# Kernel optimization log

Measured on AMD Instinct MI355X. Metric: run time of the kernel, lower is better.

The kernel has to match this reference:

```python
import math
import jax, jax.numpy as jnp
import numpy as np

B, L, D, H = 4, 1024, 512, 8
DK = D // H

def setup_inputs() -> dict:
    key = jax.random.key(0)
    ks = jax.random.split(key, 12)
    s = 0.02
    return {
        "query": jax.random.normal(ks[0], (B, L, D), jnp.float32),
        "key": jax.random.normal(ks[1], (B, L, D), jnp.float32),
        "value": jax.random.normal(ks[2], (B, L, D), jnp.float32),
        "wq_w": jax.random.normal(ks[3], (D, D), jnp.float32) * s,
        "wq_b": jnp.zeros((D,), jnp.float32),
        "wk_w": jax.random.normal(ks[4], (D, D), jnp.float32) * s,
        "wk_b": jnp.zeros((D,), jnp.float32),
        "wv_w": jax.random.normal(ks[5], (D, D), jnp.float32) * s,
        "wv_b": jnp.zeros((D,), jnp.float32),
        "dense_w": jax.random.normal(ks[6], (D, D), jnp.float32) * s,
        "dense_b": jnp.zeros((D,), jnp.float32),
        "gate_w": jax.random.normal(ks[7], (D, 1), jnp.float32) * s,
        "gate_b": jnp.zeros((1,), jnp.float32),
        "mp_wq_w": jax.random.normal(ks[8], (D, D), jnp.float32) * s,
        "mp_wq_b": jnp.zeros((D,), jnp.float32),
        "mp_wk_w": jax.random.normal(ks[9], (D, D), jnp.float32) * s,
        "mp_wk_b": jnp.zeros((D,), jnp.float32),
    }

def reference(query, key, value, wq_w, wq_b, wk_w, wk_b, wv_w, wv_b,
              dense_w, dense_b, gate_w, gate_b,
              mp_wq_w, mp_wq_b, mp_wk_w, mp_wk_b):
    # Multi-head projections -> (B, H, L, DK)
    q = (query @ wq_w + wq_b).reshape(B, L, H, DK).transpose(0, 2, 1, 3)
    k = (key @ wk_w + wk_b).reshape(B, L, H, DK).transpose(0, 2, 1, 3)
    v = (value @ wv_w + wv_b).reshape(B, L, H, DK).transpose(0, 2, 1, 3)

    # MaskPerturbation on original (unprojected-into-heads) Q, K; scale by sqrt(d_model)
    qp = query @ mp_wq_w + mp_wq_b              # (B, L, D)
    kp = key @ mp_wk_w + mp_wk_b                # (B, L, D)
    m = jax.nn.sigmoid(jnp.einsum('bqd,bkd->bqk', qp, kp) / math.sqrt(D))  # (B, L, L)

    # Scaled dot-product attention (no mask)
    scores = jnp.einsum('bhqd,bhkd->bhqk', q, k) / math.sqrt(DK)  # (B, H, L, L)
    p_attn = jax.nn.softmax(scores, axis=-1)

    # Calibration: attn_cal = attn * exp(1 - m), combined with per-query gate, re-softmax
    attn_cal = p_attn * jnp.exp(1.0 - m[:, None])                 # (B, H, L, L)
    g = jax.nn.sigmoid(query @ gate_w + gate_b)[:, None]          # (B, 1, L, 1)
    attn_comb = g * p_attn + (1.0 - g) * attn_cal
    attn_final = jax.nn.softmax(attn_comb, axis=-1)

    out = jnp.einsum('bhqk,bhkd->bhqd', attn_final, v)            # (B, H, L, DK)
    out = out.transpose(0, 2, 1, 3).reshape(B, L, D)
    out = out @ dense_w + dense_b                                 # dropout p=0 (eval)
    return (out, m)
```

## Files before the change

### kernel.cpp

```cpp
#include <hip/hip_runtime.h>

#define B_  4
#define L_  1024
#define D_  512
#define H_  8
#define DK_ 64
#define BL_ (B_*L_)

typedef unsigned short us16;
typedef __attribute__((ext_vector_type(8))) short bf16x8;
typedef __attribute__((ext_vector_type(4))) float f32x4;

__device__ __forceinline__ float us2f(us16 u) {
  union { unsigned int i; float f; } x;
  x.i = ((unsigned int)u) << 16;
  return x.f;
}
__device__ __forceinline__ us16 f2us(float f) {
  union { float f; unsigned int i; } x;
  x.f = f;
  unsigned int r = x.i + 0x7FFFu + ((x.i >> 16) & 1u);
  return (us16)(r >> 16);
}
__device__ __forceinline__ us16 cvt_us(float f) { return f2us(f); }
__device__ __forceinline__ us16 cvt_us(us16 u) { return u; }
__device__ __forceinline__ float fexp2(float x) {
  return __builtin_amdgcn_exp2f(x);
}

#define MFMA(a, b, c) __builtin_amdgcn_mfma_f32_16x16x32_bf16(a, b, c, 0, 0, 0)

struct WT6 {
  const float* src[6];
  us16* dst[6];
};
__global__ __launch_bounds__(256) void wtrans6(WT6 p) {
  __shared__ us16 T[64][72];
  const int z = blockIdx.z;
  const float* __restrict__ W = p.src[z];
  us16* __restrict__ Wt = p.dst[z];
  const int t = threadIdx.x;
  const int k0 = blockIdx.y * 64, n0 = blockIdx.x * 64;
  {
    int r = t >> 2, c = (t & 3) * 16;
    const float* src = W + (size_t)(k0 + r) * 512 + n0 + c;
    union { bf16x8 v; us16 u[8]; } p0, p1;
#pragma unroll
    for (int j = 0; j < 8; ++j) { p0.u[j] = f2us(src[j]); p1.u[j] = f2us(src[8 + j]); }
    *(bf16x8*)&T[r][c] = p0.v;
    *(bf16x8*)&T[r][c + 8] = p1.v;
  }
  __syncthreads();
  {
    int n = t >> 2, c = (t & 3) * 16;
    union { bf16x8 v; us16 u[8]; } p0, p1;
#pragma unroll
    for (int j = 0; j < 8; ++j) { p0.u[j] = T[c + j][n]; p1.u[j] = T[c + 8 + j][n]; }
    us16* dst = Wt + (size_t)(n0 + n) * 512 + k0 + c;
    *(bf16x8*)dst = p0.v;
    *(bf16x8*)(dst + 8) = p1.v;
  }
}

struct GJob { const float* A; const us16* Wt; const float* bias; us16* C; int mode; };
struct GJobs { GJob j[3]; };

__global__ __launch_bounds__(256) void gemm3(GJobs jobs) {
  __shared__ us16 Al[64][72];
  __shared__ us16 Wl[64][72];
  int f = blockIdx.x + 8 * (blockIdx.y + 64 * blockIdx.z);
  const int cpx = 64 * (int)gridDim.z;
  f = (f & 7) * cpx + (f >> 3);
  const int bx = f & 7, by = (f >> 3) & 63, bz = f >> 9;
  const GJob J = jobs.j[bz];
  const int tid = threadIdx.x;
  const int w = tid >> 6, lane = tid & 63;
  const int quad = lane >> 4, lc = lane & 15;
  const int row0 = by * 64, col0 = bx * 64;
  const int sr = tid >> 2, sc = (tid & 3) * 16;
  f32x4 acc[4] = {};
  for (int k0 = 0; k0 < 512; k0 += 64) {
    {
      const float* as = J.A + (size_t)(row0 + sr) * 512 + k0 + sc;
      union { bf16x8 v; us16 u[8]; } p0, p1;
#pragma unroll
      for (int j = 0; j < 8; ++j) { p0.u[j] = f2us(as[j]); p1.u[j] = f2us(as[8 + j]); }
      *(bf16x8*)&Al[sr][sc] = p0.v;
      *(bf16x8*)&Al[sr][sc + 8] = p1.v;
    }
    {
      const us16* wsrc = J.Wt + (size_t)(col0 + sr) * 512 + k0 + sc;
      *(bf16x8*)&Wl[sr][sc] = *(const bf16x8*)wsrc;
      *(bf16x8*)&Wl[sr][sc + 8] = *(const bf16x8*)(wsrc + 8);
    }
    __syncthreads();
    bf16x8 a0 = *(const bf16x8*)&Al[w * 16 + lc][quad * 8];
    bf16x8 a1 = *(const bf16x8*)&Al[w * 16 + lc][32 + quad * 8];
#pragma unroll
    for (int ct = 0; ct < 4; ++ct) {
      bf16x8 b0 = *(const bf16x8*)&Wl[ct * 16 + lc][quad * 8];
      bf16x8 b1 = *(const bf16x8*)&Wl[ct * 16 + lc][32 + quad * 8];
      acc[ct] = MFMA(a0, b0, acc[ct]);
      acc[ct] = MFMA(a1, b1, acc[ct]);
    }
    __syncthreads();
  }
  const int orow = row0 + w * 16 + quad * 4;
#pragma unroll
  for (int ct = 0; ct < 4; ++ct) {
    const int col = col0 + ct * 16 + lc;
    const float bv = J.bias[col];
    if (J.mode == 0) {
#pragma unroll
      for (int r = 0; r < 4; ++r)
        J.C[(size_t)(orow + r) * 512 + col] = f2us(acc[ct][r] + bv);
    } else {
      const int h = col >> 6, dk = col & 63;
#pragma unroll
      for (int r = 0; r < 4; ++r) {
        const int grow = orow + r;
        const int b = grow >> 10, kv = grow & 1023;
        J.C[(((size_t)b * H_ + h) * DK_ + dk) * L_ + kv] = f2us(acc[ct][r] + bv);
      }
    }
  }
}

__global__ __launch_bounds__(256) void gemm_dense(
    const us16* __restrict__ A, const us16* __restrict__ Wt,
    const float* __restrict__ bias, float* __restrict__ C) {
  __shared__ us16 Al[64][72];
  __shared__ us16 Wl[64][72];
  int f = blockIdx.x + 8 * blockIdx.y;
  f = (f & 7) * 64 + (f >> 3);
  const int bx = f & 7, by = f >> 3;
  const int tid = threadIdx.x;
  const int w = tid >> 6, lane = tid & 63;
  const int quad = lane >> 4, lc = lane & 15;
  const int row0 = by * 64, col0 = bx * 64;
  const int sr = tid >> 2, sc = (tid & 3) * 16;
  f32x4 acc[4] = {};
  for (int k0 = 0; k0 < 512; k0 += 64) {
    const us16* as = A + (size_t)(row0 + sr) * 512 + k0 + sc;
    const us16* wsrc = Wt + (size_t)(col0 + sr) * 512 + k0 + sc;
    *(bf16x8*)&Al[sr][sc] = *(const bf16x8*)as;
    *(bf16x8*)&Al[sr][sc + 8] = *(const bf16x8*)(as + 8);
    *(bf16x8*)&Wl[sr][sc] = *(const bf16x8*)wsrc;
    *(bf16x8*)&Wl[sr][sc + 8] = *(const bf16x8*)(wsrc + 8);
    __syncthreads();
    bf16x8 a0 = *(const bf16x8*)&Al[w * 16 + lc][quad * 8];
    bf16x8 a1 = *(const bf16x8*)&Al[w * 16 + lc][32 + quad * 8];
#pragma unroll
    for (int ct = 0; ct < 4; ++ct) {
      bf16x8 b0 = *(const bf16x8*)&Wl[ct * 16 + lc][quad * 8];
      bf16x8 b1 = *(const bf16x8*)&Wl[ct * 16 + lc][32 + quad * 8];
      acc[ct] = MFMA(a0, b0, acc[ct]);
      acc[ct] = MFMA(a1, b1, acc[ct]);
    }
    __syncthreads();
  }
  const int orow = row0 + w * 16 + quad * 4;
#pragma unroll
  for (int ct = 0; ct < 4; ++ct) {
    const int col = col0 + ct * 16 + lc;
    const float bv = bias[col];
#pragma unroll
    for (int r = 0; r < 4; ++r)
      C[(size_t)(orow + r) * 512 + col] = acc[ct][r] + bv;
  }
}

__global__ __launch_bounds__(256) void gate_kernel(
    const float* __restrict__ query, const float* __restrict__ gw,
    const float* __restrict__ gb, float* __restrict__ g) {
  int row = blockIdx.x * 4 + (threadIdx.x >> 6);
  int lane = threadIdx.x & 63;
  float p = 0.f;
  for (int d = lane; d < D_; d += 64) p += query[(size_t)row * D_ + d] * gw[d];
#pragma unroll
  for (int off = 32; off; off >>= 1) p += __shfl_down(p, off);
  if (lane == 0) g[row] = 1.f / (1.f + __expf(-(p + gb[0])));
}

template <bool WK>
__global__ __launch_bounds__(256) void mask16(
    const us16* __restrict__ QP, const us16* __restrict__ KP,
    float* __restrict__ Mout, const float* __restrict__ gbuf,
    us16* __restrict__ Wk) {
  __shared__ us16 Al[64][56];
  __shared__ us16 Bl[64][56];
  int f = blockIdx.x + 16 * (blockIdx.y + 16 * blockIdx.z);
  f = (f & 7) * 128 + (f >> 3);
  const int bx = f & 15, by = (f >> 4) & 15, b = f >> 8;
  const int tid = threadIdx.x;
  const int w = tid >> 6, lane = tid & 63;
  const int quad = lane >> 4, lc = lane & 15;
  const int row0 = by * 64, col0 = bx * 64;
  const us16* Ab = QP + (size_t)b * L_ * D_;
  const us16* Bb = KP + (size_t)b * L_ * D_;
  f32x4 acc[4] = {};
  const int arow = tid >> 2, aks = (tid & 3) * 8;
  for (int k0 = 0; k0 < 512; k0 += 32) {
    *(bf16x8*)&Al[arow][aks] =
        *(const bf16x8*)(Ab + (size_t)(row0 + arow) * 512 + k0 + aks);
    *(bf16x8*)&Bl[arow][aks] =
        *(const bf16x8*)(Bb + (size_t)(col0 + arow) * 512 + k0 + aks);
    __syncthreads();
    bf16x8 af = *(const bf16x8*)&Al[w * 16 + lc][quad * 8];
#pragma unroll
    for (int ct = 0; ct < 4; ++ct) {
      bf16x8 bf = *(const bf16x8*)&Bl[ct * 16 + lc][quad * 8];
      acc[ct] = MFMA(af, bf, acc[ct]);
    }
    __syncthreads();
  }
  const float sc = 0.04419417382415922f;
  const int orow = row0 + w * 16 + quad * 4;
  float gq[4];
  if (WK) {
#pragma unroll
    for (int r = 0; r < 4; ++r) gq[r] = gbuf[b * L_ + orow + r];
  }
#pragma unroll
  for (int ct = 0; ct < 4; ++ct) {
    const int col = col0 + ct * 16 + lc;
#pragma unroll
    for (int r = 0; r < 4; ++r) {
      float x = acc[ct][r] * sc;
      float v = 1.f / (1.f + __expf(-x));
      size_t idx = ((size_t)b * L_ + orow + r) * L_ + col;
      Mout[idx] = v;
      if (WK) Wk[idx] = f2us(gq[r] + (1.f - gq[r]) * __expf(1.f - v));
    }
  }
}

__global__ __launch_bounds__(256, 4) void attn5(
    const us16* Qp, const us16* __restrict__ Kp,
    const us16* __restrict__ Vt, const us16* __restrict__ Wk, us16* O) {
  __shared__ us16 P[16 * 1032];
  __shared__ float red[2][4][16];
  const int tid = threadIdx.x;
  const int w = tid >> 6, lane = tid & 63;
  const int quad = lane >> 4, lc = lane & 15;
  int f = blockIdx.x + 64 * (blockIdx.y + 8 * blockIdx.z);
  f = (f & 7) * 256 + (f >> 3);
  const int q0 = (f & 63) * 16;
  const int h = (f >> 6) & 7;
  const int b = f >> 9;

  const us16* qptr = Qp + (size_t)(b * L_ + q0 + lc) * D_ + h * DK_;
  bf16x8 qa0 = *(const bf16x8*)(qptr + quad * 8);
  bf16x8 qa1 = *(const bf16x8*)(qptr + 32 + quad * 8);

  const us16* Kbase = Kp + (size_t)b * L_ * D_ + h * DK_;
  const float c1 = 0.18033688011112042f;

  float s[16][4];
  float sm[4] = {0.f, 0.f, 0.f, 0.f};
#pragma unroll
  for (int kt = 0; kt < 16; ++kt) {
    const us16* kr = Kbase + (size_t)(kt * 64 + w * 16 + lc) * D_;
    bf16x8 b0 = *(const bf16x8*)(kr + quad * 8);
    bf16x8 b1 = *(const bf16x8*)(kr + 32 + quad * 8);
    f32x4 a = {};
    __builtin_amdgcn_s_setprio(1);
    a = MFMA(qa0, b0, a);
    a = MFMA(qa1, b1, a);
    __builtin_amdgcn_s_setprio(0);
#pragma unroll
    for (int r = 0; r < 4; ++r) {
      float e = fexp2(a[r] * c1);
      s[kt][r] = e;
      sm[r] += e;
    }
  }
#pragma unroll
  for (int r = 0; r < 4; ++r)
#pragma unroll
    for (int off = 1; off < 16; off <<= 1) sm[r] += __shfl_xor(sm[r], off);
  if (lc == 0)
#pragma unroll
    for (int r = 0; r < 4; ++r) red[0][w][quad * 4 + r] = sm[r];
  __syncthreads();
  float invr[4];
#pragma unroll
  for (int r = 0; r < 4; ++r) {
    const int row = quad * 4 + r;
    invr[r] = 1.44269504088896341f /
              (red[0][0][row] + red[0][1][row] + red[0][2][row] + red[0][3][row]);
  }

  const us16* wkb = Wk + (size_t)(b * L_ + q0 + quad * 4) * L_ + w * 16 + lc;
  float ts[4] = {0.f, 0.f, 0.f, 0.f};
#pragma unroll
  for (int kt = 0; kt < 16; ++kt) {
#pragma unroll
    for (int r = 0; r < 4; ++r) {
      float cv = s[kt][r] * invr[r] * us2f(wkb[(size_t)r * L_ + kt * 64]);
      float e2 = fexp2(cv);
      ts[r] += e2;
      P[(quad * 4 + r) * 1032 + kt * 64 + w * 16 + lc] = f2us(e2);
    }
  }
#pragma unroll
  for (int r = 0; r < 4; ++r)
#pragma unroll
    for (int off = 1; off < 16; off <<= 1) ts[r] += __shfl_xor(ts[r], off);
  if (lc == 0)
#pragma unroll
    for (int r = 0; r < 4; ++r) red[1][w][quad * 4 + r] = ts[r];
  __syncthreads();

  const us16* Vb = Vt + ((size_t)(b * H_ + h) * DK_ + w * 16 + lc) * L_;
  f32x4 oacc = {};
  for (int kv = 0; kv < L_; kv += 32) {
    bf16x8 pa = *(const bf16x8*)&P[lc * 1032 + kv + quad * 8];
    bf16x8 vb = *(const bf16x8*)(Vb + kv + quad * 8);
    __builtin_amdgcn_s_setprio(1);
    oacc = MFMA(pa, vb, oacc);
    __builtin_amdgcn_s_setprio(0);
  }
#pragma unroll
  for (int r = 0; r < 4; ++r) {
    const int row = quad * 4 + r;
    float inv2 = 1.f /
        (red[1][0][row] + red[1][1][row] + red[1][2][row] + red[1][3][row]);
    O[(size_t)(b * L_ + q0 + row) * D_ + h * DK_ + w * 16 + lc] =
        f2us(oacc[r] * inv2);
  }
}

template <int MODE, typename TA>
__global__ __launch_bounds__(256) void gemm16(
    const TA* __restrict__ A, const float* __restrict__ W,
    const float* __restrict__ bias, void* __restrict__ Cout) {
  __shared__ us16 Al[64][56];
  __shared__ us16 Wl[64][56];
  const int tid = threadIdx.x;
  const int w = tid >> 6, lane = tid & 63;
  const int quad = lane >> 4, lc = lane & 15;
  const int row0 = blockIdx.y * 64, col0 = blockIdx.x * 64;
  f32x4 acc[4] = {};
  const int arow = tid >> 2, aks = (tid & 3) * 8;
  const int wk = tid & 31, wns = (tid >> 5) * 8;
  for (int k0 = 0; k0 < 512; k0 += 32) {
    {
      union { bf16x8 v; us16 u[8]; } pk;
      const TA* src = A + (size_t)(row0 + arow) * 512 + k0 + aks;
#pragma unroll
      for (int j = 0; j < 8; ++j) pk.u[j] = cvt_us(src[j]);
      *(bf16x8*)&Al[arow][aks] = pk.v;
    }
    {
      const float* src = W + (size_t)(k0 + wk) * 512 + col0 + wns;
#pragma unroll
      for (int j = 0; j < 8; ++j) Wl[wns + j][wk] = f2us(src[j]);
    }
    __syncthreads();
    bf16x8 af = *(const bf16x8*)&Al[w * 16 + lc][quad * 8];
#pragma unroll
    for (int ct = 0; ct < 4; ++ct) {
      bf16x8 bf = *(const bf16x8*)&Wl[ct * 16 + lc][quad * 8];
      acc[ct] = MFMA(af, bf, acc[ct]);
    }
    __syncthreads();
  }
  const int orow = row0 + w * 16 + quad * 4;
#pragma unroll
  for (int ct = 0; ct < 4; ++ct) {
    const int col = col0 + ct * 16 + lc;
    const float bv = bias[col];
    if (MODE == 0) {
      us16* C = (us16*)Cout;
#pragma unroll
      for (int r = 0; r < 4; ++r)
        C[(size_t)(orow + r) * 512 + col] = f2us(acc[ct][r] + bv);
    } else if (MODE == 1) {
      us16* C = (us16*)Cout;
      const int h = col >> 6, dk = col & 63;
#pragma unroll
      for (int r = 0; r < 4; ++r) {
        const int grow = orow + r;
        const int b = grow >> 10, kv = grow & 1023;
        C[(((size_t)b * H_ + h) * DK_ + dk) * L_ + kv] = f2us(acc[ct][r] + bv);
      }
    } else {
      float* C = (float*)Cout;
#pragma unroll
      for (int r = 0; r < 4; ++r)
        C[(size_t)(orow + r) * 512 + col] = acc[ct][r] + bv;
    }
  }
}

__global__ __launch_bounds__(256, 3) void attn2_fb(
    const us16* Qp, const us16* __restrict__ Kp,
    const us16* __restrict__ Vt, const float* __restrict__ Mm,
    const float* __restrict__ gbuf, us16* O) {
  __shared__ us16 Ql[16][72];
  __shared__ us16 P[16 * 1032];
  __shared__ float red[2][4][16];
  const int tid = threadIdx.x;
  const int w = tid >> 6, lane = tid & 63;
  const int quad = lane >> 4, lc = lane & 15;
  const int b = blockIdx.z, h = blockIdx.y, q0 = blockIdx.x * 16;
  if (tid < 128) {
    int r = tid >> 3, ks = (tid & 7) * 8;
    *(bf16x8*)&Ql[r][ks] =
        *(const bf16x8*)(Qp + (size_t)(b * L_ + q0 + r) * D_ + h * DK_ + ks);
  }
  __syncthreads();
  bf16x8 qa0 = *(const bf16x8*)&Ql[lc][quad * 8];
  bf16x8 qa1 = *(const bf16x8*)&Ql[lc][32 + quad * 8];
  const us16* Kbase = Kp + (size_t)b * L_ * D_ + h * DK_;
  float s[16][4];
#pragma unroll
  for (int kt = 0; kt < 16; ++kt) {
    const us16* kr = Kbase + (size_t)(kt * 64 + w * 16 + lc) * D_;
    bf16x8 b0 = *(const bf16x8*)(kr + quad * 8);
    bf16x8 b1 = *(const bf16x8*)(kr + 32 + quad * 8);
    f32x4 a = {};
    a = MFMA(qa0, b0, a);
    a = MFMA(qa1, b1, a);
#pragma unroll
    for (int r = 0; r < 4; ++r) s[kt][r] = a[r] * 0.125f;
  }
  float sm[4];
#pragma unroll
  for (int r = 0; r < 4; ++r) {
    float t = 0.f;
#pragma unroll
    for (int kt = 0; kt < 16; ++kt) { s[kt][r] = __expf(s[kt][r]); t += s[kt][r]; }
#pragma unroll
    for (int off = 1; off < 16; off <<= 1) t += __shfl_xor(t, off);
    sm[r] = t;
  }
  if (lc == 0)
#pragma unroll
    for (int r = 0; r < 4; ++r) red[0][w][quad * 4 + r] = sm[r];
  __syncthreads();
  float inv[4];
#pragma unroll
  for (int r = 0; r < 4; ++r) {
    const int row = quad * 4 + r;
    inv[r] = 1.f / (red[0][0][row] + red[0][1][row] + red[0][2][row] + red[0][3][row]);
  }
  float gq[4];
#pragma unroll
  for (int r = 0; r < 4; ++r) gq[r] = gbuf[b * L_ + q0 + quad * 4 + r];
#pragma unroll
  for (int r = 0; r < 4; ++r) {
    const float* mrow = Mm + (size_t)(b * L_ + q0 + quad * 4 + r) * L_;
    float t = 0.f;
#pragma unroll
    for (int kt = 0; kt < 16; ++kt) {
      float mval = mrow[kt * 64 + w * 16 + lc];
      float c = s[kt][r] * inv[r] * (gq[r] + (1.f - gq[r]) * __expf(1.f - mval));
      float e = __expf(c);
      s[kt][r] = e;
      t += e;
    }
#pragma unroll
    for (int off = 1; off < 16; off <<= 1) t += __shfl_xor(t, off);
    sm[r] = t;
  }
  if (lc == 0)
#pragma unroll
    for (int r = 0; r < 4; ++r) red[1][w][quad * 4 + r] = sm[r];
  __syncthreads();
#pragma unroll
  for (int r = 0; r < 4; ++r) {
    const int row = quad * 4 + r;
    inv[r] = 1.f / (red[1][0][row] + red[1][1][row] + red[1][2][row] + red[1][3][row]);
  }
#pragma unroll
  for (int kt = 0; kt < 16; ++kt)
#pragma unroll
    for (int r = 0; r < 4; ++r)
      P[(quad * 4 + r) * 1032 + kt * 64 + w * 16 + lc] = f2us(s[kt][r] * inv[r]);
  __syncthreads();
  const us16* Vb = Vt + (size_t)(b * H_ + h) * DK_ * L_;
  f32x4 oacc = {};
  for (int kv = 0; kv < L_; kv += 32) {
    bf16x8 pa = *(const bf16x8*)&P[lc * 1032 + kv + quad * 8];
    bf16x8 vb = *(const bf16x8*)(Vb + (size_t)(w * 16 + lc) * L_ + kv + quad * 8);
    oacc = MFMA(pa, vb, oacc);
  }
#pragma unroll
  for (int r = 0; r < 4; ++r)
    O[(size_t)(b * L_ + q0 + quad * 4 + r) * D_ + h * DK_ + w * 16 + lc] =
        f2us(oacc[r]);
}

extern "C" void kernel_launch(void* const* d_in, const int* in_sizes, int n_in,
                              void* d_out, int out_size, void* d_ws, size_t ws_size,
                              hipStream_t stream) {
  const float* query   = (const float*)d_in[0];
  const float* key     = (const float*)d_in[1];
  const float* value   = (const float*)d_in[2];
  const float* wq_w    = (const float*)d_in[3];
  const float* wq_b    = (const float*)d_in[4];
  const float* wk_w    = (const float*)d_in[5];
  const float* wk_b    = (const float*)d_in[6];
  const float* wv_w    = (const float*)d_in[7];
  const float* wv_b    = (const float*)d_in[8];
  const float* dense_w = (const float*)d_in[9];
  const float* dense_b = (const float*)d_in[10];
  const float* gate_w  = (const float*)d_in[11];
  const float* gate_b  = (const float*)d_in[12];
  const float* mp_wq_w = (const float*)d_in[13];
  const float* mp_wq_b = (const float*)d_in[14];
  const float* mp_wk_w = (const float*)d_in[15];
  const float* mp_wk_b = (const float*)d_in[16];

  const size_t RSZ = (size_t)BL_ * D_;
  const size_t WSZ = (size_t)D_ * D_;
  us16* R0 = (us16*)d_ws;
  us16* R1 = R0 + RSZ;

  float* out0 = (float*)d_out;
  float* outm = out0 + (size_t)B_ * L_ * D_;
  us16*  Vt   = (us16*)d_out;
  float* gbuf = (float*)((char*)d_out + (4u << 20));

  dim3 blk(256);
  dim3 gattn(L_ / 16, H_, B_);

  if (ws_size >= ((size_t)20 << 20)) {
    us16* Wt0 = R1 + RSZ;
    us16* mpq_t = Wt0;
    us16* mpk_t = Wt0 + WSZ;
    us16* wq_t  = Wt0 + 2 * WSZ;
    us16* wk_t  = Wt0 + 3 * WSZ;
    us16* wv_t  = Wt0 + 4 * WSZ;
    us16* dw_t  = Wt0 + 5 * WSZ;
    us16* Wk    = Wt0 + 6 * WSZ;

    WT6 wt;
    wt.src[0] = mp_wq_w; wt.dst[0] = mpq_t;
    wt.src[1] = mp_wk_w; wt.dst[1] = mpk_t;
    wt.src[2] = wq_w;    wt.dst[2] = wq_t;
    wt.src[3] = wk_w;    wt.dst[3] = wk_t;
    wt.src[4] = wv_w;    wt.dst[4] = wv_t;
    wt.src[5] = dense_w; wt.dst[5] = dw_t;
    hipLaunchKernelGGL(wtrans6, dim3(8, 8, 6), blk, 0, stream, wt);
    hipLaunchKernelGGL(gate_kernel, dim3(BL_ / 4), blk, 0, stream, query, gate_w, gate_b, gbuf);

    GJobs mp;
    mp.j[0] = { query, mpq_t, mp_wq_b, R0, 0 };
    mp.j[1] = { key,   mpk_t, mp_wk_b, R1, 0 };
    mp.j[2] = mp.j[1];
    hipLaunchKernelGGL(gemm3, dim3(8, 64, 2), blk, 0, stream, mp);
    hipLaunchKernelGGL(mask16<true>, dim3(16, 16, B_), blk, 0, stream,
                       R0, R1, outm, gbuf, Wk);

    GJobs qkv;
    qkv.j[0] = { query, wq_t, wq_b, R0, 0 };
    qkv.j[1] = { key,   wk_t, wk_b, R1, 0 };
    qkv.j[2] = { value, wv_t, wv_b, Vt, 1 };
    hipLaunchKernelGGL(gemm3, dim3(8, 64, 3), blk, 0, stream, qkv);

    hipLaunchKernelGGL(attn5, gattn, blk, 0, stream, R0, R1, Vt, Wk, R0);
    hipLaunchKernelGGL(gemm_dense, dim3(8, 64), blk, 0, stream, R0, dw_t, dense_b, out0);
  } else {
    dim3 gproj(8, 64);
    hipLaunchKernelGGL((gemm16<0, float>), gproj, blk, 0, stream, query, mp_wq_w, mp_wq_b, (void*)R0);
    hipLaunchKernelGGL((gemm16<0, float>), gproj, blk, 0, stream, key,   mp_wk_w, mp_wk_b, (void*)R1);
    hipLaunchKernelGGL(mask16<false>, dim3(16, 16, B_), blk, 0, stream,
                       R0, R1, outm, (const float*)nullptr, (us16*)nullptr);
    hipLaunchKernelGGL((gemm16<0, float>), gproj, blk, 0, stream, query, wq_w, wq_b, (void*)R0);
    hipLaunchKernelGGL((gemm16<0, float>), gproj, blk, 0, stream, key,   wk_w, wk_b, (void*)R1);
    hipLaunchKernelGGL((gemm16<1, float>), gproj, blk, 0, stream, value, wv_w, wv_b, (void*)Vt);
    hipLaunchKernelGGL(gate_kernel, dim3(BL_ / 4), blk, 0, stream, query, gate_w, gate_b, gbuf);
    hipLaunchKernelGGL(attn2_fb, gattn, blk, 0, stream, R0, R1, Vt, outm, gbuf, R0);
    hipLaunchKernelGGL((gemm16<2, us16>), gproj, blk, 0, stream, R0, dense_w, dense_b, (void*)out0);
  }
}
```

Baseline: 240.0 us.

## Split attention key range across two warp groups with 512-thread blocks

The attention kernel now runs 512 threads per block, with two groups of four warps each covering half of the key dimension. Each group keeps half as many score registers, writes its own P slice, and the PV partial sums are combined through shared memory before normalization. The aim is more parallelism and less register pressure per query tile, at the cost of an extra barrier and a cross-group reduction.

```diff
diff --git a/kernel.cpp b/kernel.cpp
--- a/kernel.cpp
+++ b/kernel.cpp
@@ -235,13 +235,15 @@
   }
 }
 
-__global__ __launch_bounds__(256, 4) void attn5(
+__global__ __launch_bounds__(512, 6) void attn6(
     const us16* Qp, const us16* __restrict__ Kp,
     const us16* __restrict__ Vt, const us16* __restrict__ Wk, us16* O) {
-  __shared__ us16 P[16 * 1032];
-  __shared__ float red[2][4][16];
+  __shared__ us16 P[2][16][520];
+  __shared__ float xacc[4][16][16];
+  __shared__ float red[2][8][16];
   const int tid = threadIdx.x;
-  const int w = tid >> 6, lane = tid & 63;
+  const int W = tid >> 6, lane = tid & 63;
+  const int g = W >> 2, w = W & 3;
   const int quad = lane >> 4, lc = lane & 15;
   int f = blockIdx.x + 64 * (blockIdx.y + 8 * blockIdx.z);
   f = (f & 7) * 256 + (f >> 3);
@@ -253,14 +255,15 @@
   bf16x8 qa0 = *(const bf16x8*)(qptr + quad * 8);
   bf16x8 qa1 = *(const bf16x8*)(qptr + 32 + quad * 8);
 
-  const us16* Kbase = Kp + (size_t)b * L_ * D_ + h * DK_;
+  const us16* Kbase = Kp + (size_t)b * L_ * D_ + h * DK_ +
+                      (size_t)(g * 512 + w * 16 + lc) * D_;
   const float c1 = 0.18033688011112042f;
 
-  float s[16][4];
+  float s[8][4];
   float sm[4] = {0.f, 0.f, 0.f, 0.f};
 #pragma unroll
-  for (int kt = 0; kt < 16; ++kt) {
-    const us16* kr = Kbase + (size_t)(kt * 64 + w * 16 + lc) * D_;
+  for (int kk = 0; kk < 8; ++kk) {
+    const us16* kr = Kbase + (size_t)(kk * 64) * D_;
     bf16x8 b0 = *(const bf16x8*)(kr + quad * 8);
     bf16x8 b1 = *(const bf16x8*)(kr + 32 + quad * 8);
     f32x4 a = {};
@@ -271,7 +274,7 @@
 #pragma unroll
     for (int r = 0; r < 4; ++r) {
       float e = fexp2(a[r] * c1);
-      s[kt][r] = e;
+      s[kk][r] = e;
       sm[r] += e;
     }
   }
@@ -281,26 +284,29 @@
     for (int off = 1; off < 16; off <<= 1) sm[r] += __shfl_xor(sm[r], off);
   if (lc == 0)
 #pragma unroll
-    for (int r = 0; r < 4; ++r) red[0][w][quad * 4 + r] = sm[r];
+    for (int r = 0; r < 4; ++r) red[0][W][quad * 4 + r] = sm[r];
   __syncthreads();
   float invr[4];
 #pragma unroll
   for (int r = 0; r < 4; ++r) {
     const int row = quad * 4 + r;
-    invr[r] = 1.44269504088896341f /
-              (red[0][0][row] + red[0][1][row] + red[0][2][row] + red[0][3][row]);
-  }
-
-  const us16* wkb = Wk + (size_t)(b * L_ + q0 + quad * 4) * L_ + w * 16 + lc;
+    float t = 0.f;
+#pragma unroll
+    for (int j = 0; j < 8; ++j) t += red[0][j][row];
+    invr[r] = 1.44269504088896341f / t;
+  }
+
+  const us16* wkb = Wk + (size_t)(b * L_ + q0 + quad * 4) * L_ +
+                    g * 512 + w * 16 + lc;
   float ts[4] = {0.f, 0.f, 0.f, 0.f};
 #pragma unroll
-  for (int kt = 0; kt < 16; ++kt) {
+  for (int kk = 0; kk < 8; ++kk) {
 #pragma unroll
     for (int r = 0; r < 4; ++r) {
-      float cv = s[kt][r] * invr[r] * us2f(wkb[(size_t)r * L_ + kt * 64]);
+      float cv = s[kk][r] * invr[r] * us2f(wkb[(size_t)r * L_ + kk * 64]);
       float e2 = fexp2(cv);
       ts[r] += e2;
-      P[(quad * 4 + r) * 1032 + kt * 64 + w * 16 + lc] = f2us(e2);
+      P[g][quad * 4 + r][kk * 64 + w * 16 + lc] = f2us(e2);
     }
   }
 #pragma unroll
@@ -309,25 +315,35 @@
     for (int off = 1; off < 16; off <<= 1) ts[r] += __shfl_xor(ts[r], off);
   if (lc == 0)
 #pragma unroll
-    for (int r = 0; r < 4; ++r) red[1][w][quad * 4 + r] = ts[r];
-  __syncthreads();
-
-  const us16* Vb = Vt + ((size_t)(b * H_ + h) * DK_ + w * 16 + lc) * L_;
+    for (int r = 0; r < 4; ++r) red[1][W][quad * 4 + r] = ts[r];
+  __syncthreads();
+
+  const us16* Vb = Vt + ((size_t)(b * H_ + h) * DK_ + w * 16 + lc) * L_ +
+                   g * 512;
   f32x4 oacc = {};
-  for (int kv = 0; kv < L_; kv += 32) {
-    bf16x8 pa = *(const bf16x8*)&P[lc * 1032 + kv + quad * 8];
+#pragma unroll
+  for (int kv = 0; kv < 512; kv += 32) {
+    bf16x8 pa = *(const bf16x8*)&P[g][lc][kv + quad * 8];
     bf16x8 vb = *(const bf16x8*)(Vb + kv + quad * 8);
     __builtin_amdgcn_s_setprio(1);
     oacc = MFMA(pa, vb, oacc);
     __builtin_amdgcn_s_setprio(0);
   }
-#pragma unroll
-  for (int r = 0; r < 4; ++r) {
-    const int row = quad * 4 + r;
-    float inv2 = 1.f /
-        (red[1][0][row] + red[1][1][row] + red[1][2][row] + red[1][3][row]);
-    O[(size_t)(b * L_ + q0 + row) * D_ + h * DK_ + w * 16 + lc] =
-        f2us(oacc[r] * inv2);
+  if (g == 1) {
+#pragma unroll
+    for (int r = 0; r < 4; ++r) xacc[w][quad * 4 + r][lc] = oacc[r];
+  }
+  __syncthreads();
+  if (g == 0) {
+#pragma unroll
+    for (int r = 0; r < 4; ++r) {
+      const int row = quad * 4 + r;
+      float t = 0.f;
+#pragma unroll
+      for (int j = 0; j < 8; ++j) t += red[1][j][row];
+      float o = (oacc[r] + xacc[w][row][lc]) / t;
+      O[(size_t)(b * L_ + q0 + row) * D_ + h * DK_ + w * 16 + lc] = f2us(o);
+    }
   }
 }
 
@@ -561,7 +577,7 @@
     qkv.j[2] = { value, wv_t, wv_b, Vt, 1 };
     hipLaunchKernelGGL(gemm3, dim3(8, 64, 3), blk, 0, stream, qkv);
 
-    hipLaunchKernelGGL(attn5, gattn, blk, 0, stream, R0, R1, Vt, Wk, R0);
+    hipLaunchKernelGGL(attn6, gattn, dim3(512), 0, stream, R0, R1, Vt, Wk, R0);
     hipLaunchKernelGGL(gemm_dense, dim3(8, 64), blk, 0, stream, R0, dw_t, dense_b, out0);
   } else {
     dim3 gproj(8, 64);
```

Measured after the change: 245.7 us. 1.02x slower.

## Enlarge GEMM tiles to 128x64, fuse gate into weight prep, remap block swizzles

Applied to the files above, without the earlier changes.

The projection GEMMs, the dense GEMM and the mask GEMM now use 128-row tiles, with each wave computing two 16-row MFMA tiles, so every B fragment is reused twice and the grids are halved. The mask kernel also moves from a K-step of 32 to 64. The gate computation is folded into the weight-transpose kernel as extra blocks, saving one launch. Block-index swizzles are rewritten for the new grid shapes (attn5 included), presumably to spread blocks across XCDs. The cost is more LDS and registers per block and fewer blocks in flight.

```diff
diff --git a/kernel.cpp b/kernel.cpp
--- a/kernel.cpp
+++ b/kernel.cpp
@@ -34,13 +34,27 @@
   const float* src[6];
   us16* dst[6];
 };
-__global__ __launch_bounds__(256) void wtrans6(WT6 p) {
+__global__ __launch_bounds__(256) void prep(WT6 p, const float* __restrict__ query,
+    const float* __restrict__ gw, const float* __restrict__ gb,
+    float* __restrict__ g) {
   __shared__ us16 T[64][72];
-  const int z = blockIdx.z;
+  int id = blockIdx.x;
+  if (id < 1024) {
+    int row = id * 4 + (threadIdx.x >> 6);
+    int lane = threadIdx.x & 63;
+    float pz = 0.f;
+    for (int d = lane; d < D_; d += 64) pz += query[(size_t)row * D_ + d] * gw[d];
+#pragma unroll
+    for (int off = 32; off; off >>= 1) pz += __shfl_down(pz, off);
+    if (lane == 0) g[row] = 1.f / (1.f + __expf(-(pz + gb[0])));
+    return;
+  }
+  id -= 1024;
+  const int z = id >> 6;
+  const int k0 = ((id >> 3) & 7) * 64, n0 = (id & 7) * 64;
   const float* __restrict__ W = p.src[z];
   us16* __restrict__ Wt = p.dst[z];
   const int t = threadIdx.x;
-  const int k0 = blockIdx.y * 64, n0 = blockIdx.x * 64;
   {
     int r = t >> 2, c = (t & 3) * 16;
     const float* src = W + (size_t)(k0 + r) * 512 + n0 + c;
@@ -59,114 +73,6 @@
     us16* dst = Wt + (size_t)(n0 + n) * 512 + k0 + c;
     *(bf16x8*)dst = p0.v;
     *(bf16x8*)(dst + 8) = p1.v;
-  }
-}
-
-struct GJob { const float* A; const us16* Wt; const float* bias; us16* C; int mode; };
-struct GJobs { GJob j[3]; };
-
-__global__ __launch_bounds__(256) void gemm3(GJobs jobs) {
-  __shared__ us16 Al[64][72];
-  __shared__ us16 Wl[64][72];
-  int f = blockIdx.x + 8 * (blockIdx.y + 64 * blockIdx.z);
-  const int cpx = 64 * (int)gridDim.z;
-  f = (f & 7) * cpx + (f >> 3);
-  const int bx = f & 7, by = (f >> 3) & 63, bz = f >> 9;
-  const GJob J = jobs.j[bz];
-  const int tid = threadIdx.x;
-  const int w = tid >> 6, lane = tid & 63;
-  const int quad = lane >> 4, lc = lane & 15;
-  const int row0 = by * 64, col0 = bx * 64;
-  const int sr = tid >> 2, sc = (tid & 3) * 16;
-  f32x4 acc[4] = {};
-  for (int k0 = 0; k0 < 512; k0 += 64) {
-    {
-      const float* as = J.A + (size_t)(row0 + sr) * 512 + k0 + sc;
-      union { bf16x8 v; us16 u[8]; } p0, p1;
-#pragma unroll
-      for (int j = 0; j < 8; ++j) { p0.u[j] = f2us(as[j]); p1.u[j] = f2us(as[8 + j]); }
-      *(bf16x8*)&Al[sr][sc] = p0.v;
-      *(bf16x8*)&Al[sr][sc + 8] = p1.v;
-    }
-    {
-      const us16* wsrc = J.Wt + (size_t)(col0 + sr) * 512 + k0 + sc;
-      *(bf16x8*)&Wl[sr][sc] = *(const bf16x8*)wsrc;
-      *(bf16x8*)&Wl[sr][sc + 8] = *(const bf16x8*)(wsrc + 8);
-    }
-    __syncthreads();
-    bf16x8 a0 = *(const bf16x8*)&Al[w * 16 + lc][quad * 8];
-    bf16x8 a1 = *(const bf16x8*)&Al[w * 16 + lc][32 + quad * 8];
-#pragma unroll
-    for (int ct = 0; ct < 4; ++ct) {
-      bf16x8 b0 = *(const bf16x8*)&Wl[ct * 16 + lc][quad * 8];
-      bf16x8 b1 = *(const bf16x8*)&Wl[ct * 16 + lc][32 + quad * 8];
-      acc[ct] = MFMA(a0, b0, acc[ct]);
-      acc[ct] = MFMA(a1, b1, acc[ct]);
-    }
-    __syncthreads();
-  }
-  const int orow = row0 + w * 16 + quad * 4;
-#pragma unroll
-  for (int ct = 0; ct < 4; ++ct) {
-    const int col = col0 + ct * 16 + lc;
-    const float bv = J.bias[col];
-    if (J.mode == 0) {
-#pragma unroll
-      for (int r = 0; r < 4; ++r)
-        J.C[(size_t)(orow + r) * 512 + col] = f2us(acc[ct][r] + bv);
-    } else {
-      const int h = col >> 6, dk = col & 63;
-#pragma unroll
-      for (int r = 0; r < 4; ++r) {
-        const int grow = orow + r;
-        const int b = grow >> 10, kv = grow & 1023;
-        J.C[(((size_t)b * H_ + h) * DK_ + dk) * L_ + kv] = f2us(acc[ct][r] + bv);
-      }
-    }
-  }
-}
-
-__global__ __launch_bounds__(256) void gemm_dense(
-    const us16* __restrict__ A, const us16* __restrict__ Wt,
-    const float* __restrict__ bias, float* __restrict__ C) {
-  __shared__ us16 Al[64][72];
-  __shared__ us16 Wl[64][72];
-  int f = blockIdx.x + 8 * blockIdx.y;
-  f = (f & 7) * 64 + (f >> 3);
-  const int bx = f & 7, by = f >> 3;
-  const int tid = threadIdx.x;
-  const int w = tid >> 6, lane = tid & 63;
-  const int quad = lane >> 4, lc = lane & 15;
-  const int row0 = by * 64, col0 = bx * 64;
-  const int sr = tid >> 2, sc = (tid & 3) * 16;
-  f32x4 acc[4] = {};
-  for (int k0 = 0; k0 < 512; k0 += 64) {
-    const us16* as = A + (size_t)(row0 + sr) * 512 + k0 + sc;
-    const us16* wsrc = Wt + (size_t)(col0 + sr) * 512 + k0 + sc;
-    *(bf16x8*)&Al[sr][sc] = *(const bf16x8*)as;
-    *(bf16x8*)&Al[sr][sc + 8] = *(const bf16x8*)(as + 8);
-    *(bf16x8*)&Wl[sr][sc] = *(const bf16x8*)wsrc;
-    *(bf16x8*)&Wl[sr][sc + 8] = *(const bf16x8*)(wsrc + 8);
-    __syncthreads();
-    bf16x8 a0 = *(const bf16x8*)&Al[w * 16 + lc][quad * 8];
-    bf16x8 a1 = *(const bf16x8*)&Al[w * 16 + lc][32 + quad * 8];
-#pragma unroll
-    for (int ct = 0; ct < 4; ++ct) {
-      bf16x8 b0 = *(const bf16x8*)&Wl[ct * 16 + lc][quad * 8];
-      bf16x8 b1 = *(const bf16x8*)&Wl[ct * 16 + lc][32 + quad * 8];
-      acc[ct] = MFMA(a0, b0, acc[ct]);
-      acc[ct] = MFMA(a1, b1, acc[ct]);
-    }
-    __syncthreads();
-  }
-  const int orow = row0 + w * 16 + quad * 4;
-#pragma unroll
-  for (int ct = 0; ct < 4; ++ct) {
-    const int col = col0 + ct * 16 + lc;
-    const float bv = bias[col];
-#pragma unroll
-    for (int r = 0; r < 4; ++r)
-      C[(size_t)(orow + r) * 512 + col] = acc[ct][r] + bv;
   }
 }
 
@@ -182,55 +88,227 @@
   if (lane == 0) g[row] = 1.f / (1.f + __expf(-(p + gb[0])));
 }
 
+struct GJob { const float* A; const us16* Wt; const float* bias; us16* C; int mode; };
+struct GJobs { GJob j[3]; };
+
+__global__ __launch_bounds__(256) void gemm3(GJobs jobs) {
+  __shared__ us16 Al[128][72];
+  __shared__ us16 Wl[64][72];
+  const int nz = (int)gridDim.z;
+  int raw = blockIdx.x + 8 * (blockIdx.y + 32 * blockIdx.z);
+  const int c = raw & 7;
+  const int rest = raw >> 3;
+  const int pg = 4 * nz;
+  const int bx = rest / pg;
+  const int pp = c * pg + rest % pg;
+  const int by = pp & 31, bz = pp >> 5;
+  const GJob J = jobs.j[bz];
+  const int tid = threadIdx.x;
+  const int w = tid >> 6, lane = tid & 63;
+  const int quad = lane >> 4, lc = lane & 15;
+  const int row0 = by * 128, col0 = bx * 64;
+  const int asr = tid >> 1, asc = (tid & 1) * 32;
+  const int bsr = tid >> 2, bsc = (tid & 3) * 16;
+  f32x4 acc[2][4] = {};
+  for (int k0 = 0; k0 < 512; k0 += 64) {
+    {
+      const float* as = J.A + (size_t)(row0 + asr) * 512 + k0 + asc;
+      union { bf16x8 v; us16 u[8]; } q0, q1, q2, q3;
+#pragma unroll
+      for (int j = 0; j < 8; ++j) {
+        q0.u[j] = f2us(as[j]);       q1.u[j] = f2us(as[8 + j]);
+        q2.u[j] = f2us(as[16 + j]);  q3.u[j] = f2us(as[24 + j]);
+      }
+      *(bf16x8*)&Al[asr][asc]      = q0.v;
+      *(bf16x8*)&Al[asr][asc + 8]  = q1.v;
+      *(bf16x8*)&Al[asr][asc + 16] = q2.v;
+      *(bf16x8*)&Al[asr][asc + 24] = q3.v;
+    }
+    {
+      const us16* wsrc = J.Wt + (size_t)(col0 + bsr) * 512 + k0 + bsc;
+      *(bf16x8*)&Wl[bsr][bsc]     = *(const bf16x8*)wsrc;
+      *(bf16x8*)&Wl[bsr][bsc + 8] = *(const bf16x8*)(wsrc + 8);
+    }
+    __syncthreads();
+    bf16x8 a[2][2];
+#pragma unroll
+    for (int rt = 0; rt < 2; ++rt) {
+      a[rt][0] = *(const bf16x8*)&Al[w * 32 + rt * 16 + lc][quad * 8];
+      a[rt][1] = *(const bf16x8*)&Al[w * 32 + rt * 16 + lc][32 + quad * 8];
+    }
+#pragma unroll
+    for (int ct = 0; ct < 4; ++ct) {
+      bf16x8 b0 = *(const bf16x8*)&Wl[ct * 16 + lc][quad * 8];
+      bf16x8 b1 = *(const bf16x8*)&Wl[ct * 16 + lc][32 + quad * 8];
+#pragma unroll
+      for (int rt = 0; rt < 2; ++rt) {
+        acc[rt][ct] = MFMA(a[rt][0], b0, acc[rt][ct]);
+        acc[rt][ct] = MFMA(a[rt][1], b1, acc[rt][ct]);
+      }
+    }
+    __syncthreads();
+  }
+#pragma unroll
+  for (int rt = 0; rt < 2; ++rt) {
+    const int orow = row0 + w * 32 + rt * 16 + quad * 4;
+#pragma unroll
+    for (int ct = 0; ct < 4; ++ct) {
+      const int col = col0 + ct * 16 + lc;
+      const float bv = J.bias[col];
+      if (J.mode == 0) {
+#pragma unroll
+        for (int r = 0; r < 4; ++r)
+          J.C[(size_t)(orow + r) * 512 + col] = f2us(acc[rt][ct][r] + bv);
+      } else {
+        const int h = col >> 6, dk = col & 63;
+#pragma unroll
+        for (int r = 0; r < 4; ++r) {
+          const int grow = orow + r;
+          const int b = grow >> 10, kv = grow & 1023;
+          J.C[(((size_t)b * H_ + h) * DK_ + dk) * L_ + kv] = f2us(acc[rt][ct][r] + bv);
+        }
+      }
+    }
+  }
+}
+
+__global__ __launch_bounds__(256) void gemm_dense(
+    const us16* __restrict__ A, const us16* __restrict__ Wt,
+    const float* __restrict__ bias, float* __restrict__ C) {
+  __shared__ us16 Al[128][72];
+  __shared__ us16 Wl[64][72];
+  int raw = blockIdx.x + 8 * blockIdx.y;
+  const int c = raw & 7;
+  const int rest = raw >> 3;
+  const int bx = rest >> 2;
+  const int by = c * 4 + (rest & 3);
+  const int tid = threadIdx.x;
+  const int w = tid >> 6, lane = tid & 63;
+  const int quad = lane >> 4, lc = lane & 15;
+  const int row0 = by * 128, col0 = bx * 64;
+  const int asr = tid >> 1, asc = (tid & 1) * 32;
+  const int bsr = tid >> 2, bsc = (tid & 3) * 16;
+  f32x4 acc[2][4] = {};
+  for (int k0 = 0; k0 < 512; k0 += 64) {
+    {
+      const us16* as = A + (size_t)(row0 + asr) * 512 + k0 + asc;
+      *(bf16x8*)&Al[asr][asc]      = *(const bf16x8*)as;
+      *(bf16x8*)&Al[asr][asc + 8]  = *(const bf16x8*)(as + 8);
+      *(bf16x8*)&Al[asr][asc + 16] = *(const bf16x8*)(as + 16);
+      *(bf16x8*)&Al[asr][asc + 24] = *(const bf16x8*)(as + 24);
+    }
+    {
+      const us16* wsrc = Wt + (size_t)(col0 + bsr) * 512 + k0 + bsc;
+      *(bf16x8*)&Wl[bsr][bsc]     = *(const bf16x8*)wsrc;
+      *(bf16x8*)&Wl[bsr][bsc + 8] = *(const bf16x8*)(wsrc + 8);
+    }
+    __syncthreads();
+    bf16x8 a[2][2];
+#pragma unroll
+    for (int rt = 0; rt < 2; ++rt) {
+      a[rt][0] = *(const bf16x8*)&Al[w * 32 + rt * 16 + lc][quad * 8];
+      a[rt][1] = *(const bf16x8*)&Al[w * 32 + rt * 16 + lc][32 + quad * 8];
+    }
+#pragma unroll
+    for (int ct = 0; ct < 4; ++ct) {
+      bf16x8 b0 = *(const bf16x8*)&Wl[ct * 16 + lc][quad * 8];
+      bf16x8 b1 = *(const bf16x8*)&Wl[ct * 16 + lc][32 + quad * 8];
+#pragma unroll
+      for (int rt = 0; rt < 2; ++rt) {
+        acc[rt][ct] = MFMA(a[rt][0], b0, acc[rt][ct]);
+        acc[rt][ct] = MFMA(a[rt][1], b1, acc[rt][ct]);
+      }
+    }
+    __syncthreads();
+  }
+#pragma unroll
+  for (int rt = 0; rt < 2; ++rt) {
+    const int orow = row0 + w * 32 + rt * 16 + quad * 4;
+#pragma unroll
+    for (int ct = 0; ct < 4; ++ct) {
+      const int col = col0 + ct * 16 + lc;
+      const float bv = bias[col];
+#pragma unroll
+      for (int r = 0; r < 4; ++r)
+        C[(size_t)(orow + r) * 512 + col] = acc[rt][ct][r] + bv;
+    }
+  }
+}
+
 template <bool WK>
 __global__ __launch_bounds__(256) void mask16(
     const us16* __restrict__ QP, const us16* __restrict__ KP,
     float* __restrict__ Mout, const float* __restrict__ gbuf,
     us16* __restrict__ Wk) {
-  __shared__ us16 Al[64][56];
-  __shared__ us16 Bl[64][56];
-  int f = blockIdx.x + 16 * (blockIdx.y + 16 * blockIdx.z);
-  f = (f & 7) * 128 + (f >> 3);
-  const int bx = f & 15, by = (f >> 4) & 15, b = f >> 8;
+  __shared__ us16 Al[128][72];
+  __shared__ us16 Bl[64][72];
+  int raw = blockIdx.x + 16 * (blockIdx.y + 8 * blockIdx.z);
+  const int c = raw & 7;
+  const int rest = raw >> 3;
+  const int cx = rest >> 2;
+  const int gg = c * 4 + (rest & 3);
+  const int ry = gg & 7, b = gg >> 3;
   const int tid = threadIdx.x;
   const int w = tid >> 6, lane = tid & 63;
   const int quad = lane >> 4, lc = lane & 15;
-  const int row0 = by * 64, col0 = bx * 64;
+  const int row0 = ry * 128, col0 = cx * 64;
   const us16* Ab = QP + (size_t)b * L_ * D_;
   const us16* Bb = KP + (size_t)b * L_ * D_;
-  f32x4 acc[4] = {};
-  const int arow = tid >> 2, aks = (tid & 3) * 8;
-  for (int k0 = 0; k0 < 512; k0 += 32) {
-    *(bf16x8*)&Al[arow][aks] =
-        *(const bf16x8*)(Ab + (size_t)(row0 + arow) * 512 + k0 + aks);
-    *(bf16x8*)&Bl[arow][aks] =
-        *(const bf16x8*)(Bb + (size_t)(col0 + arow) * 512 + k0 + aks);
-    __syncthreads();
-    bf16x8 af = *(const bf16x8*)&Al[w * 16 + lc][quad * 8];
+  const int asr = tid >> 1, asc = (tid & 1) * 32;
+  const int bsr = tid >> 2, bsc = (tid & 3) * 16;
+  f32x4 acc[2][4] = {};
+  for (int k0 = 0; k0 < 512; k0 += 64) {
+    {
+      const us16* as = Ab + (size_t)(row0 + asr) * 512 + k0 + asc;
+      *(bf16x8*)&Al[asr][asc]      = *(const bf16x8*)as;
+      *(bf16x8*)&Al[asr][asc + 8]  = *(const bf16x8*)(as + 8);
+      *(bf16x8*)&Al[asr][asc + 16] = *(const bf16x8*)(as + 16);
+      *(bf16x8*)&Al[asr][asc + 24] = *(const bf16x8*)(as + 24);
+    }
+    {
+      const us16* bs = Bb + (size_t)(col0 + bsr) * 512 + k0 + bsc;
+      *(bf16x8*)&Bl[bsr][bsc]     = *(const bf16x8*)bs;
+      *(bf16x8*)&Bl[bsr][bsc + 8] = *(const bf16x8*)(bs + 8);
+    }
+    __syncthreads();
+    bf16x8 a[2][2];
+#pragma unroll
+    for (int rt = 0; rt < 2; ++rt) {
+      a[rt][0] = *(const bf16x8*)&Al[w * 32 + rt * 16 + lc][quad * 8];
+      a[rt][1] = *(const bf16x8*)&Al[w * 32 + rt * 16 + lc][32 + quad * 8];
+    }
 #pragma unroll
     for (int ct = 0; ct < 4; ++ct) {
-      bf16x8 bf = *(const bf16x8*)&Bl[ct * 16 + lc][quad * 8];
-      acc[ct] = MFMA(af, bf, acc[ct]);
+      bf16x8 b0 = *(const bf16x8*)&Bl[ct * 16 + lc][quad * 8];
+      bf16x8 b1 = *(const bf16x8*)&Bl[ct * 16 + lc][32 + quad * 8];
+#pragma unroll
+      for (int rt = 0; rt < 2; ++rt) {
+        acc[rt][ct] = MFMA(a[rt][0], b0, acc[rt][ct]);
+        acc[rt][ct] = MFMA(a[rt][1], b1, acc[rt][ct]);
+      }
     }
     __syncthreads();
   }
   const float sc = 0.04419417382415922f;
-  const int orow = row0 + w * 16 + quad * 4;
-  float gq[4];
-  if (WK) {
-#pragma unroll
-    for (int r = 0; r < 4; ++r) gq[r] = gbuf[b * L_ + orow + r];
-  }
-#pragma unroll
-  for (int ct = 0; ct < 4; ++ct) {
-    const int col = col0 + ct * 16 + lc;
-#pragma unroll
-    for (int r = 0; r < 4; ++r) {
-      float x = acc[ct][r] * sc;
-      float v = 1.f / (1.f + __expf(-x));
-      size_t idx = ((size_t)b * L_ + orow + r) * L_ + col;
-      Mout[idx] = v;
-      if (WK) Wk[idx] = f2us(gq[r] + (1.f - gq[r]) * __expf(1.f - v));
+#pragma unroll
+  for (int rt = 0; rt < 2; ++rt) {
+    const int orow = row0 + w * 32 + rt * 16 + quad * 4;
+    float gq[4];
+    if (WK) {
+#pragma unroll
+      for (int r = 0; r < 4; ++r) gq[r] = gbuf[b * L_ + orow + r];
+    }
+#pragma unroll
+    for (int ct = 0; ct < 4; ++ct) {
+      const int col = col0 + ct * 16 + lc;
+#pragma unroll
+      for (int r = 0; r < 4; ++r) {
+        float x = acc[rt][ct][r] * sc;
+        float v = 1.f / (1.f + __expf(-x));
+        size_t idx = ((size_t)b * L_ + orow + r) * L_ + col;
+        Mout[idx] = v;
+        if (WK) Wk[idx] = f2us(gq[r] + (1.f - gq[r]) * __expf(1.f - v));
+      }
     }
   }
 }
@@ -243,11 +321,12 @@
   const int tid = threadIdx.x;
   const int w = tid >> 6, lane = tid & 63;
   const int quad = lane >> 4, lc = lane & 15;
-  int f = blockIdx.x + 64 * (blockIdx.y + 8 * blockIdx.z);
-  f = (f & 7) * 256 + (f >> 3);
-  const int q0 = (f & 63) * 16;
-  const int h = (f >> 6) & 7;
-  const int b = f >> 9;
+  int raw = blockIdx.x + 64 * (blockIdx.y + 8 * blockIdx.z);
+  const int c = raw & 7;
+  const int rest = raw >> 3;
+  const int gg = c * 4 + (rest & 3);
+  const int q0 = (rest >> 2) * 16;
+  const int h = gg & 7, b = gg >> 3;
 
   const us16* qptr = Qp + (size_t)(b * L_ + q0 + lc) * D_ + h * DK_;
   bf16x8 qa0 = *(const bf16x8*)(qptr + quad * 8);
@@ -525,7 +604,6 @@
   float* gbuf = (float*)((char*)d_out + (4u << 20));
 
   dim3 blk(256);
-  dim3 gattn(L_ / 16, H_, B_);
 
   if (ws_size >= ((size_t)20 << 20)) {
     us16* Wt0 = R1 + RSZ;
@@ -544,36 +622,35 @@
     wt.src[3] = wk_w;    wt.dst[3] = wk_t;
     wt.src[4] = wv_w;    wt.dst[4] = wv_t;
     wt.src[5] = dense_w; wt.dst[5] = dw_t;
-    hipLaunchKernelGGL(wtrans6, dim3(8, 8, 6), blk, 0, stream, wt);
-    hipLaunchKernelGGL(gate_kernel, dim3(BL_ / 4), blk, 0, stream, query, gate_w, gate_b, gbuf);
+    hipLaunchKernelGGL(prep, dim3(1408), blk, 0, stream, wt, query, gate_w, gate_b, gbuf);
 
     GJobs mp;
     mp.j[0] = { query, mpq_t, mp_wq_b, R0, 0 };
     mp.j[1] = { key,   mpk_t, mp_wk_b, R1, 0 };
     mp.j[2] = mp.j[1];
-    hipLaunchKernelGGL(gemm3, dim3(8, 64, 2), blk, 0, stream, mp);
-    hipLaunchKernelGGL(mask16<true>, dim3(16, 16, B_), blk, 0, stream,
+    hipLaunchKernelGGL(gemm3, dim3(8, 32, 2), blk, 0, stream, mp);
+    hipLaunchKernelGGL(mask16<true>, dim3(16, 8, B_), blk, 0, stream,
                        R0, R1, outm, gbuf, Wk);
 
     GJobs qkv;
     qkv.j[0] = { query, wq_t, wq_b, R0, 0 };
     qkv.j[1] = { key,   wk_t, wk_b, R1, 0 };
     qkv.j[2] = { value, wv_t, wv_b, Vt, 1 };
-    hipLaunchKernelGGL(gemm3, dim3(8, 64, 3), blk, 0, stream, qkv);
-
-    hipLaunchKernelGGL(attn5, gattn, blk, 0, stream, R0, R1, Vt, Wk, R0);
-    hipLaunchKernelGGL(gemm_dense, dim3(8, 64), blk, 0, stream, R0, dw_t, dense_b, out0);
+    hipLaunchKernelGGL(gemm3, dim3(8, 32, 3), blk, 0, stream, qkv);
+
+    hipLaunchKernelGGL(attn5, dim3(L_ / 16, H_, B_), blk, 0, stream, R0, R1, Vt, Wk, R0);
+    hipLaunchKernelGGL(gemm_dense, dim3(8, 32), blk, 0, stream, R0, dw_t, dense_b, out0);
   } else {
     dim3 gproj(8, 64);
     hipLaunchKernelGGL((gemm16<0, float>), gproj, blk, 0, stream, query, mp_wq_w, mp_wq_b, (void*)R0);
     hipLaunchKernelGGL((gemm16<0, float>), gproj, blk, 0, stream, key,   mp_wk_w, mp_wk_b, (void*)R1);
-    hipLaunchKernelGGL(mask16<false>, dim3(16, 16, B_), blk, 0, stream,
+    hipLaunchKernelGGL(mask16<false>, dim3(16, 8, B_), blk, 0, stream,
                        R0, R1, outm, (const float*)nullptr, (us16*)nullptr);
     hipLaunchKernelGGL((gemm16<0, float>), gproj, blk, 0, stream, query, wq_w, wq_b, (void*)R0);
     hipLaunchKernelGGL((gemm16<0, float>), gproj, blk, 0, stream, key,   wk_w, wk_b, (void*)R1);
     hipLaunchKernelGGL((gemm16<1, float>), gproj, blk, 0, stream, value, wv_w, wv_b, (void*)Vt);
     hipLaunchKernelGGL(gate_kernel, dim3(BL_ / 4), blk, 0, stream, query, gate_w, gate_b, gbuf);
-    hipLaunchKernelGGL(attn2_fb, gattn, blk, 0, stream, R0, R1, Vt, outm, gbuf, R0);
+    hipLaunchKernelGGL(attn2_fb, dim3(L_ / 16, H_, B_), blk, 0, stream, R0, R1, Vt, outm, gbuf, R0);
     hipLaunchKernelGGL((gemm16<2, us16>), gproj, blk, 0, stream, R0, dense_w, dense_b, (void*)out0);
   }
 }
```

After: 263.1 us. 1.1x slower.
